# Kernel tuning notes

Hardware: AMD Instinct MI355X
Metric: run time of the kernel (lower is better)

## Reference

```python
import jax, jax.numpy as jnp
import numpy as np

B, S = 2, 2048
D_MODEL = 1024
N_HEADS = 16
N_VALUES = 8192
D_RETR = 128
MAX_POS = 2048


def setup_inputs() -> dict:
    key = jax.random.key(0)
    ks = jax.random.split(key, 10)
    s = 0.02
    return {
        "hidden_states": jax.random.normal(ks[0], (B, S, D_MODEL), jnp.float32),
        "attention_mask": jnp.ones((B, S), jnp.float32),
        "Wq": jax.random.normal(ks[1], (D_MODEL, D_MODEL), jnp.float32) * s,
        "bq": jnp.zeros((D_MODEL,), jnp.float32),
        "Wk": jax.random.normal(ks[2], (D_MODEL, D_MODEL), jnp.float32) * s,
        "bk": jnp.zeros((D_MODEL,), jnp.float32),
        # torch init is round(ones)=all ones; use random 0/1 so the per-head dynamic mask is exercised
        "dynamic_mask": jnp.round(jax.random.uniform(ks[3], (N_HEADS, MAX_POS), jnp.float32)),
        "Wvq": jax.random.normal(ks[4], (D_MODEL, D_RETR), jnp.float32) * s,
        "bvq": jnp.zeros((D_RETR,), jnp.float32),
        "v_keys": jax.random.normal(ks[5], (N_VALUES, D_RETR), jnp.float32) * s,
        "v_embed": jax.random.normal(ks[6], (N_VALUES, D_MODEL), jnp.float32) * s,
        "Wo": jax.random.normal(ks[7], (D_MODEL, D_MODEL), jnp.float32) * s,
        "bo": jnp.zeros((D_MODEL,), jnp.float32),
    }


def reference(hidden_states, attention_mask, Wq, bq, Wk, bk, dynamic_mask,
              Wvq, bvq, v_keys, v_embed, Wo, bo):
    b, s, d = hidden_states.shape
    h = dynamic_mask.shape[0]
    hd = d // h
    dtype = hidden_states.dtype
    min_d = jnp.finfo(dtype).min

    q = (hidden_states @ Wq + bq).reshape(b, s, h, hd).transpose(0, 2, 1, 3)  # [B,H,S,hd]
    k = (hidden_states @ Wk + bk).reshape(b, s, h, hd).transpose(0, 2, 1, 3)

    # inner_func: top-1 codebook value retrieval
    vq = hidden_states @ Wvq + bvq                      # [B,S,Dr]
    sim = jnp.einsum('bsr,nr->bsn', vq, v_keys)         # [B,S,Nv]
    idx = jnp.argmax(sim, axis=-1)                      # top-1 indices [B,S]
    v = hidden_states * v_embed[idx]                    # [B,S,D]
    v = v.reshape(b, s, h, hd).transpose(0, 2, 1, 3)    # [B,H,S,hd]

    # 4D causal mask fused with per-head dynamic mask and padding mask
    tgt = attention_mask.shape[-1]
    causal = jnp.where(jnp.arange(tgt)[None, :] > jnp.arange(s)[:, None],
                       min_d, jnp.array(0, dtype))[None, None]        # [1,1,S,S]
    am = attention_mask[:, None, None, :] * dynamic_mask[None, :, None, :tgt]  # [B,H,1,S]
    padding = causal + am                                              # [B,H,S,S]
    mask = jnp.where(padding == 0, min_d, causal)                      # [B,H,S,S]

    scores = jnp.einsum('bhqd,bhkd->bhqk', q, k) / jnp.sqrt(jnp.array(hd, dtype))
    scores = scores + mask
    w = jax.nn.softmax(scores.astype(jnp.float32), axis=-1).astype(dtype)

    out = jnp.einsum('bhqk,bhkd->bhqd', w, v)            # [B,H,S,hd]
    out = out.transpose(0, 2, 1, 3).reshape(b, s, d)
    return out @ Wo + bo
```

## Files before the change

kernel.cpp:

```cpp
#include <hip/hip_runtime.h>
#include <hip/hip_bf16.h>
#include <math.h>

#define MIN_D (-3.402823466e+38f)

constexpr int Bb = 2, Ss = 2048, Dm = 1024, Hh = 16, HDd = 64, NV = 8192, DRr = 128;
constexpr int Mrows = Bb * Ss;
constexpr float MARGIN = 0.01f;
constexpr int CAP = 262144;
constexpr float C2 = 0.18033688011112042f;

typedef __attribute__((ext_vector_type(8))) short bf16x8;
typedef __attribute__((ext_vector_type(4))) float f32x4;

__device__ inline unsigned short f2bf(float x) {
    union { float f; unsigned u; } v; v.f = x;
    unsigned r = v.u + 0x7fff + ((v.u >> 16) & 1);
    return (unsigned short)(r >> 16);
}
__device__ inline float bf2f(unsigned short u) {
    union { unsigned u; float f; } v; v.u = ((unsigned)u) << 16;
    return v.f;
}
__device__ inline unsigned pk_bf16(float a, float b) {
    float2 t; t.x = a; t.y = b;
    __hip_bfloat162 h = __float22bfloat162_rn(t);
    return *(unsigned*)&h;
}

__global__ __launch_bounds__(256)
void cvt_bf16(const float* __restrict__ x, unsigned short* __restrict__ y)
{
    size_t i = ((size_t)blockIdx.x * 256 + threadIdx.x) * 8;
    float4 a = *(const float4*)(x + i);
    float4 b = *(const float4*)(x + i + 4);
    uint4 p;
    p.x = pk_bf16(a.x, a.y);
    p.y = pk_bf16(a.z, a.w);
    p.z = pk_bf16(b.x, b.y);
    p.w = pk_bf16(b.z, b.w);
    *(uint4*)(y + i) = p;
}

__global__ __launch_bounds__(256)
void transpose_cvt3(const float* __restrict__ W0, const float* __restrict__ W1,
                    const float* __restrict__ W2, unsigned short* __restrict__ T0,
                    unsigned short* __restrict__ T1, unsigned short* __restrict__ T2)
{
    const float* W = blockIdx.z == 0 ? W0 : (blockIdx.z == 1 ? W1 : W2);
    unsigned short* WT = blockIdx.z == 0 ? T0 : (blockIdx.z == 1 ? T1 : T2);
    __shared__ unsigned short T[64][72];
    const int tid = threadIdx.x;
    const int n0 = blockIdx.x * 64, k0 = blockIdx.y * 64;
    const int rr = tid >> 4, cc = tid & 15;
#pragma unroll
    for (int q2 = 0; q2 < 4; ++q2) {
        int kk = rr * 4 + q2;
        float4 v = *(const float4*)(W + (size_t)(k0 + kk) * Dm + n0 + cc * 4);
        T[cc * 4 + 0][kk] = f2bf(v.x);
        T[cc * 4 + 1][kk] = f2bf(v.y);
        T[cc * 4 + 2][kk] = f2bf(v.z);
        T[cc * 4 + 3][kk] = f2bf(v.w);
    }
    __syncthreads();
#pragma unroll
    for (int q2 = 0; q2 < 4; ++q2) {
        int nn = rr * 4 + q2;
        uint2 u;
        u.x = (unsigned)T[nn][cc * 4 + 0] | ((unsigned)T[nn][cc * 4 + 1] << 16);
        u.y = (unsigned)T[nn][cc * 4 + 2] | ((unsigned)T[nn][cc * 4 + 3] << 16);
        *(uint2*)(WT + (size_t)(n0 + nn) * Dm + k0 + cc * 4) = u;
    }
}

template<bool BF16OUT>
__global__ __launch_bounds__(512)
void gemm_bf16(const unsigned short* __restrict__ A,
               const unsigned short* BT0, const unsigned short* BT1,
               const float* bias0, const float* bias1,
               void* C0, void* C1, int N, int K)
{
    const unsigned short* BT = blockIdx.z ? BT1 : BT0;
    const float* bias = blockIdx.z ? bias1 : bias0;
    void* C = blockIdx.z ? C1 : C0;
    __shared__ __align__(16) unsigned short As[128 * 32];
    __shared__ __align__(16) unsigned short Bs[128 * 32];
    const int tid = threadIdx.x;
    const int l = tid & 63, w = tid >> 6;
    const int l15 = l & 15, l4 = l >> 4;
    const int wm = w >> 2, wn = w & 3;
    const int row0 = blockIdx.y * 128, col0 = blockIdx.x * 128;

    f32x4 acc[4][2];
#pragma unroll
    for (int mi = 0; mi < 4; ++mi)
#pragma unroll
        for (int ni = 0; ni < 2; ++ni) acc[mi][ni] = (f32x4)(0.f);

    for (int k0 = 0; k0 < K; k0 += 32) {
        __syncthreads();
        {
            int r = tid >> 2, pc = tid & 3;
            uint4 vv = *(const uint4*)(A + (size_t)(row0 + r) * K + k0 + pc * 8);
            *(uint4*)&As[tid * 8] = vv;
        }
        {
            int r = tid >> 2, pc = tid & 3;
            uint4 vv = *(const uint4*)(BT + (size_t)(col0 + r) * K + k0 + pc * 8);
            *(uint4*)&Bs[tid * 8] = vv;
        }
        __syncthreads();

        bf16x8 af[4], bf[2];
#pragma unroll
        for (int mi = 0; mi < 4; ++mi)
            af[mi] = *(bf16x8*)&As[(wm * 64 + mi * 16 + l15) * 32 + l4 * 8];
#pragma unroll
        for (int ni = 0; ni < 2; ++ni)
            bf[ni] = *(bf16x8*)&Bs[(wn * 32 + ni * 16 + l15) * 32 + l4 * 8];
#pragma unroll
        for (int mi = 0; mi < 4; ++mi)
#pragma unroll
            for (int ni = 0; ni < 2; ++ni)
                acc[mi][ni] = __builtin_amdgcn_mfma_f32_16x16x32_bf16(af[mi], bf[ni], acc[mi][ni], 0, 0, 0);
    }

#pragma unroll
    for (int mi = 0; mi < 4; ++mi)
#pragma unroll
        for (int ni = 0; ni < 2; ++ni)
#pragma unroll
            for (int j = 0; j < 4; ++j) {
                int row = row0 + wm * 64 + mi * 16 + l4 * 4 + j;
                int col = col0 + wn * 32 + ni * 16 + l15;
                float vv = acc[mi][ni][j] + bias[col];
                if (BF16OUT)
                    ((unsigned short*)C)[(size_t)row * N + col] = f2bf(vv);
                else
                    ((float*)C)[(size_t)row * N + col] = vv;
            }
}

__global__ __launch_bounds__(256)
void gemm_vq_partial(const float* __restrict__ A, const float* __restrict__ W,
                     float* __restrict__ P)
{
    __shared__ float As[64][36];
    __shared__ float Ws[32][64];
    const int tid = threadIdx.x;
    const int row0 = blockIdx.y * 64, col0 = blockIdx.x * 64;
    const int kbase = blockIdx.z * 256;
    const int tr = tid >> 4, tc = tid & 15;
    float acc[4][4] = {};

    for (int k0 = kbase; k0 < kbase + 256; k0 += 32) {
        __syncthreads();
#pragma unroll
        for (int q2 = 0; q2 < 2; ++q2) {
            int oc = q2 * 256 + tid;
            int r = oc >> 3, c4 = (oc & 7) << 2;
            *(float4*)&As[r][c4] = *(const float4*)(A + (size_t)(row0 + r) * Dm + k0 + c4);
        }
#pragma unroll
        for (int q2 = 0; q2 < 2; ++q2) {
            int oc = q2 * 256 + tid;
            int r = oc >> 4, c4 = (oc & 15) << 2;
            *(float4*)&Ws[r][c4] = *(const float4*)(W + (size_t)(k0 + r) * DRr + col0 + c4);
        }
        __syncthreads();
#pragma unroll 8
        for (int kk = 0; kk < 32; ++kk) {
            float a[4];
#pragma unroll
            for (int i = 0; i < 4; ++i) a[i] = As[tr * 4 + i][kk];
            float4 bv = *(const float4*)&Ws[kk][tc * 4];
            float b[4] = {bv.x, bv.y, bv.z, bv.w};
#pragma unroll
            for (int i = 0; i < 4; ++i)
#pragma unroll
                for (int j = 0; j < 4; ++j)
                    acc[i][j] = fmaf(a[i], b[j], acc[i][j]);
        }
    }
    float* Pz = P + (size_t)blockIdx.z * Mrows * DRr;
#pragma unroll
    for (int i = 0; i < 4; ++i) {
        int r = row0 + tr * 4 + i;
        float4 ov = {acc[i][0], acc[i][1], acc[i][2], acc[i][3]};
        *(float4*)(Pz + (size_t)r * DRr + col0 + tc * 4) = ov;
    }
}

__global__ __launch_bounds__(256)
void reduce_vq(const float* __restrict__ P, const float* __restrict__ bias,
               float* __restrict__ vqb, unsigned short* __restrict__ vq_hi)
{
    const size_t i4 = ((size_t)blockIdx.x * 256 + threadIdx.x) * 4;
    const int col = (int)(i4 & 127);
    const size_t stride = (size_t)Mrows * DRr;
    float4 s = *(const float4*)(P + i4);
#pragma unroll
    for (int z = 1; z < 4; ++z) {
        float4 p = *(const float4*)(P + stride * z + i4);
        s.x += p.x; s.y += p.y; s.z += p.z; s.w += p.w;
    }
    float4 bv = *(const float4*)(bias + col);
    s.x += bv.x; s.y += bv.y; s.z += bv.z; s.w += bv.w;
    *(float4*)(vqb + i4) = s;
    uint2 u;
    u.x = pk_bf16(s.x, s.y);
    u.y = pk_bf16(s.z, s.w);
    *(uint2*)(vq_hi + i4) = u;
}

__global__ __launch_bounds__(512)
void sim_gemm0(const unsigned short* __restrict__ A,
               const unsigned short* __restrict__ BT,
               float* __restrict__ rtm)
{
    __shared__ __align__(16) unsigned short As[128 * 32];
    __shared__ __align__(16) unsigned short Bs[128 * 32];
    __shared__ float red[128][4];
    const int tid = threadIdx.x;
    const int l = tid & 63, w = tid >> 6;
    const int l15 = l & 15, l4 = l >> 4;
    const int wm = w >> 2, wn = w & 3;
    const int row0 = blockIdx.y * 128, col0 = blockIdx.x * 128;

    f32x4 acc[4][2];
#pragma unroll
    for (int mi = 0; mi < 4; ++mi)
#pragma unroll
        for (int ni = 0; ni < 2; ++ni) acc[mi][ni] = (f32x4)(0.f);

    for (int k0 = 0; k0 < DRr; k0 += 32) {
        __syncthreads();
        {
            int r = tid >> 2, pc = tid & 3;
            __builtin_amdgcn_global_load_lds(
                (const __attribute__((address_space(1))) unsigned int*)(A + (size_t)(row0 + r) * DRr + k0 + pc * 8),
                (__attribute__((address_space(3))) unsigned int*)&As[tid * 8], 16, 0, 0);
            __builtin_amdgcn_global_load_lds(
                (const __attribute__((address_space(1))) unsigned int*)(BT + (size_t)(col0 + r) * DRr + k0 + pc * 8),
                (__attribute__((address_space(3))) unsigned int*)&Bs[tid * 8], 16, 0, 0);
        }
        __syncthreads();

        bf16x8 af[4], bf[2];
#pragma unroll
        for (int mi = 0; mi < 4; ++mi)
            af[mi] = *(bf16x8*)&As[(wm * 64 + mi * 16 + l15) * 32 + l4 * 8];
#pragma unroll
        for (int ni = 0; ni < 2; ++ni)
            bf[ni] = *(bf16x8*)&Bs[(wn * 32 + ni * 16 + l15) * 32 + l4 * 8];
#pragma unroll
        for (int mi = 0; mi < 4; ++mi)
#pragma unroll
            for (int ni = 0; ni < 2; ++ni)
                acc[mi][ni] = __builtin_amdgcn_mfma_f32_16x16x32_bf16(af[mi], bf[ni], acc[mi][ni], 0, 0, 0);
    }

    float rm[4][4];
#pragma unroll
    for (int mi = 0; mi < 4; ++mi)
#pragma unroll
        for (int j = 0; j < 4; ++j)
            rm[mi][j] = fmaxf(acc[mi][0][j], acc[mi][1][j]);
#pragma unroll
    for (int off = 1; off < 16; off <<= 1)
#pragma unroll
        for (int mi = 0; mi < 4; ++mi)
#pragma unroll
            for (int j = 0; j < 4; ++j)
                rm[mi][j] = fmaxf(rm[mi][j], __shfl_xor(rm[mi][j], off));
    if (l15 == 0) {
#pragma unroll
        for (int mi = 0; mi < 4; ++mi)
#pragma unroll
            for (int j = 0; j < 4; ++j)
                red[wm * 64 + mi * 16 + l4 * 4 + j][wn] = rm[mi][j];
    }
    __syncthreads();
    if (tid < 128) {
        float m = fmaxf(fmaxf(red[tid][0], red[tid][1]),
                        fmaxf(red[tid][2], red[tid][3]));
        rtm[(size_t)blockIdx.x * Mrows + row0 + tid] = m;
    }
}

__global__ __launch_bounds__(256)
void sim_combine2(const float* __restrict__ rtm, float* __restrict__ thr)
{
    int r = blockIdx.x * 256 + threadIdx.x;
    if (r >= Mrows) return;
    float m = -INFINITY;
#pragma unroll 8
    for (int c = 0; c < 64; ++c)
        m = fmaxf(m, rtm[(size_t)c * Mrows + r]);
    thr[r] = m - MARGIN;
}

__global__ __launch_bounds__(256)
void collect_pairs(const float* __restrict__ rtm, const float* __restrict__ thr,
                   unsigned* __restrict__ cnt, unsigned* __restrict__ pairs)
{
    const int idx = blockIdx.x * 256 + threadIdx.x;
    const int tile = idx >> 12, row = idx & 4095;
    const bool pred = rtm[(size_t)tile * Mrows + row] >= thr[row];
    unsigned long long mask = __ballot(pred);
    if (mask) {
        const int lane = threadIdx.x & 63;
        const int leader = __ffsll((long long)mask) - 1;
        unsigned base = 0;
        if (lane == leader) base = atomicAdd(cnt, (unsigned)__popcll(mask));
        base = (unsigned)__shfl((int)base, leader);
        if (pred) {
            unsigned off = (unsigned)__popcll(mask & ((1ull << lane) - 1ull));
            pairs[base + off] = ((unsigned)row << 6) | (unsigned)tile;
        }
    }
}

__global__ __launch_bounds__(256)
void rescore_pair(const unsigned* __restrict__ pairs, const unsigned* __restrict__ cnt,
                  const float* __restrict__ vq, const float* __restrict__ vkeys,
                  unsigned long long* __restrict__ best)
{
    __shared__ float vqs[128];
    __shared__ float part[256];
    const int tid = threadIdx.x;
    const unsigned n = min(*cnt, (unsigned)CAP);
    for (unsigned i = blockIdx.x; i < n; i += gridDim.x) {
        const unsigned p = pairs[i];
        const unsigned row = p >> 6, tile = p & 63u;
        if (tid < 32) {
            float4 v = *(const float4*)(vq + (size_t)row * 128 + tid * 4);
            *(float4*)&vqs[tid * 4] = v;
        }
        __syncthreads();
        const int k = tid & 127, h = (tid >> 7) * 64;
        const float* kp = vkeys + (size_t)(tile * 128 + k) * 128 + h;
        float s = 0.f;
#pragma unroll
        for (int d = 0; d < 64; d += 4) {
            float4 kv = *(const float4*)(kp + d);
            s = fmaf(vqs[h + d + 0], kv.x, s);
            s = fmaf(vqs[h + d + 1], kv.y, s);
            s = fmaf(vqs[h + d + 2], kv.z, s);
            s = fmaf(vqs[h + d + 3], kv.w, s);
        }
        part[tid] = s;
        __syncthreads();
        if (tid < 64) {
            float s0 = part[tid] + part[tid + 128];
            float s1 = part[tid + 64] + part[tid + 192];
            float bs = s0; int bk = tid;
            if (s1 > s0) { bs = s1; bk = tid + 64; }
#pragma unroll
            for (int off = 1; off < 64; off <<= 1) {
                float os = __shfl_xor(bs, off);
                int ok = __shfl_xor(bk, off);
                if (os > bs || (os == bs && ok < bk)) { bs = os; bk = ok; }
            }
            if (tid == 0) {
                unsigned key = tile * 128 + bk;
                unsigned fb = __float_as_uint(bs);
                fb = (fb & 0x80000000u) ? ~fb : (fb | 0x80000000u);
                unsigned long long enc = ((unsigned long long)fb << 32) | (unsigned)(~key);
                atomicMax(best + row, enc);
            }
        }
        __syncthreads();
    }
}

__global__ __launch_bounds__(256)
void build_vt(const float* __restrict__ hs, const float* __restrict__ vembed,
              const unsigned long long* __restrict__ best,
              unsigned short* __restrict__ vt)
{
    __shared__ unsigned short T[64][73];
    __shared__ int ids[64];
    const int tid = threadIdx.x;
    const int kt = blockIdx.x;
    const int bh = blockIdx.y;
    const int b = bh >> 4, h = bh & 15;
    if (tid < 64) {
        int row = b * Ss + kt * 64 + tid;
        ids[tid] = (int)((~(unsigned)(best[row] & 0xFFFFFFFFull)) & 8191u);
    }
    __syncthreads();
    {
        int r = tid >> 2, c16 = (tid & 3) * 16;
        size_t hrow = (size_t)(b * Ss + kt * 64 + r) * Dm + h * HDd + c16;
        size_t erow = (size_t)ids[r] * Dm + h * HDd + c16;
#pragma unroll
        for (int q2 = 0; q2 < 4; ++q2) {
            float4 a = *(const float4*)(hs + hrow + q2 * 4);
            float4 e = *(const float4*)(vembed + erow + q2 * 4);
            T[r][c16 + q2 * 4 + 0] = f2bf(a.x * e.x);
            T[r][c16 + q2 * 4 + 1] = f2bf(a.y * e.y);
            T[r][c16 + q2 * 4 + 2] = f2bf(a.z * e.z);
            T[r][c16 + q2 * 4 + 3] = f2bf(a.w * e.w);
        }
    }
    __syncthreads();
    {
        int d = tid >> 2, kc = (tid & 3) * 16;
        unsigned short ob[16];
#pragma unroll
        for (int i = 0; i < 16; ++i) ob[i] = T[kc + i][d];
        unsigned short* op = vt + ((size_t)(b * Hh + h) * HDd + d) * Ss + kt * 64 + kc;
        *(uint4*)op = *(uint4*)&ob[0];
        *(uint4*)(op + 8) = *(uint4*)&ob[8];
    }
}

__global__ __launch_bounds__(256)
void mean_vt(const unsigned short* __restrict__ vt, float* __restrict__ mv)
{
    const int bh = blockIdx.x;
    const int b = bh >> 4, h = bh & 15;
    const int d = threadIdx.x >> 2, part = threadIdx.x & 3;
    const unsigned short* row = vt + ((size_t)bh * HDd + d) * Ss + part * 512;
    float s = 0.f;
    for (int j = 0; j < 512; j += 8) {
        uint4 u = *(const uint4*)(row + j);
        const unsigned uu[4] = {u.x, u.y, u.z, u.w};
#pragma unroll
        for (int m = 0; m < 4; ++m) {
            s += bf2f((unsigned short)(uu[m] & 0xffff));
            s += bf2f((unsigned short)(uu[m] >> 16));
        }
    }
    s += __shfl_xor(s, 1);
    s += __shfl_xor(s, 2);
    if (part == 0) mv[b * Dm + h * HDd + d] = s * (1.f / 2048.f);
}

__global__ __launch_bounds__(512)
void attn_mfma4(const unsigned short* __restrict__ q, const unsigned short* __restrict__ k,
                const unsigned short* __restrict__ vt, const float* __restrict__ am,
                const float* __restrict__ dmask, const float* __restrict__ meanv,
                unsigned short* __restrict__ o)
{
    __shared__ __align__(16) unsigned char smem[40960];
    __shared__ float uniflag[128];
    unsigned char* Ksm = smem;
    unsigned char* Vsm = smem + 8192;
    unsigned char* Psm = smem + 16384;
    float* amdmf = (float*)(smem + 32768);

    const int tid = threadIdx.x;
    const int l = tid & 63, w = tid >> 6;
    const int l15 = l & 15, l4 = l >> 4;
    const int lin = blockIdx.x + (blockIdx.y << 4) + (blockIdx.z << 8);
    const int half = lin >> 8, rem = lin & 255;
    const int qtb = rem & 15;
    const int qt = half ? (15 - qtb) : qtb;
    const int h = rem >> 4;
    const int b = half;
    const int row0 = qt * 128;

    {
        int j = tid * 4;
        float4 a = *(const float4*)(am + b * Ss + j);
        float4 d = *(const float4*)(dmask + h * Ss + j);
        float4 m;
        m.x = (a.x * d.x == 0.f) ? MIN_D : 0.f;
        m.y = (a.y * d.y == 0.f) ? MIN_D : 0.f;
        m.z = (a.z * d.z == 0.f) ? MIN_D : 0.f;
        m.w = (a.w * d.w == 0.f) ? MIN_D : 0.f;
        *(float4*)&amdmf[j] = m;
    }

    const int qloc = w * 16 + l15;
    const int qrow = row0 + qloc;
    bf16x8 qf[2];
    {
        const unsigned short* qp = q + ((size_t)(b * Ss + qrow)) * Dm + h * HDd + l4 * 8;
        qf[0] = *(const bf16x8*)qp;
        qf[1] = *(const bf16x8*)(qp + 32);
    }

    f32x4 acc[4];
#pragma unroll
    for (int d2 = 0; d2 < 4; ++d2) acc[d2] = (f32x4)(0.f);
    float mrun = -INFINITY, lrun = 0.f;
    const int ktmax = 2 * qt + 1;

    for (int kt = 0; kt <= ktmax; ++kt) {
        __syncthreads();
        {
            int key = tid >> 3, pc = tid & 7, lc = pc ^ (key & 7);
            uint4 vv = *(const uint4*)(k + ((size_t)(b * Ss + kt * 64 + key)) * Dm
                                       + h * HDd + lc * 8);
            *(uint4*)&Ksm[tid * 16] = vv;
        }
        {
            int d = tid >> 3, pc = tid & 7, lc = pc ^ (d & 7);
            uint4 vv = *(const uint4*)(vt + ((size_t)(b * Hh + h) * HDd + d) * Ss
                                       + kt * 64 + lc * 8);
            *(uint4*)&Vsm[tid * 16] = vv;
        }
        __syncthreads();

        f32x4 sreg[4];
#pragma unroll
        for (int kb = 0; kb < 4; ++kb) {
            const int key16 = kb * 16 + l15;
            const int sw = key16 & 7;
            bf16x8 k0 = *(bf16x8*)&Ksm[key16 * 128 + ((l4 ^ sw) * 16)];
            bf16x8 k1 = *(bf16x8*)&Ksm[key16 * 128 + (((4 + l4) ^ sw) * 16)];
            f32x4 s = (f32x4)(0.f);
            s = __builtin_amdgcn_mfma_f32_16x16x32_bf16(k0, qf[0], s, 0, 0, 0);
            s = __builtin_amdgcn_mfma_f32_16x16x32_bf16(k1, qf[1], s, 0, 0, 0);
            sreg[kb] = s;
        }

        float sv[16];
#pragma unroll
        for (int kb = 0; kb < 4; ++kb)
#pragma unroll
            for (int r = 0; r < 4; ++r) {
                const int key = kt * 64 + kb * 16 + l4 * 4 + r;
                const float mval = (key > qrow) ? MIN_D : amdmf[key];
                sv[kb * 4 + r] = fmaf(sreg[kb][r], C2, mval);
            }

        float pm = fmaxf(fmaxf(sv[0], sv[1]), sv[2]);
        pm = fmaxf(fmaxf(pm, sv[3]), fmaxf(sv[4], sv[5]));
        pm = fmaxf(fmaxf(pm, sv[6]), fmaxf(sv[7], sv[8]));
        pm = fmaxf(fmaxf(pm, sv[9]), fmaxf(sv[10], sv[11]));
        pm = fmaxf(fmaxf(pm, sv[12]), fmaxf(sv[13], sv[14]));
        pm = fmaxf(pm, sv[15]);
        pm = fmaxf(pm, __shfl_xor(pm, 16));
        pm = fmaxf(pm, __shfl_xor(pm, 32));

        if (__any(pm > mrun + 8.f)) {
            const float mn = fmaxf(mrun, pm);
            const float sc = __builtin_amdgcn_exp2f(mrun - mn);
            lrun *= sc;
#pragma unroll
            for (int d2 = 0; d2 < 4; ++d2) acc[d2] *= sc;
            mrun = mn;
        }

        float p[16], rs = 0.f;
#pragma unroll
        for (int i = 0; i < 16; ++i) {
            p[i] = __builtin_amdgcn_exp2f(sv[i] - mrun);
            rs += p[i];
        }
        rs += __shfl_xor(rs, 16);
        rs += __shfl_xor(rs, 32);
        lrun += rs;

        const unsigned pswz = (l15 & 7) << 4;
#pragma unroll
        for (int kb = 0; kb < 4; ++kb) {
            uint2 u;
            u.x = pk_bf16(p[kb * 4 + 0], p[kb * 4 + 1]);
            u.y = pk_bf16(p[kb * 4 + 2], p[kb * 4 + 3]);
            *(uint2*)&Psm[qloc * 128 + ((kb * 32 + l4 * 8) ^ pswz)] = u;
        }

#pragma unroll
        for (int ks = 0; ks < 2; ++ks) {
            bf16x8 pa = *(bf16x8*)&Psm[qloc * 128 + ((ks * 64 + l4 * 16) ^ pswz)];
#pragma unroll
            for (int d2 = 0; d2 < 4; ++d2) {
                const int dd = d2 * 16 + l15;
                bf16x8 vb = *(bf16x8*)&Vsm[dd * 128 + ((ks * 64 + l4 * 16) ^ ((dd & 7) << 4))];
                acc[d2] = __builtin_amdgcn_mfma_f32_16x16x32_bf16(vb, pa, acc[d2], 0, 0, 0);
            }
        }
    }

    const float inv = 1.f / lrun;
    const bool uni = (mrun <= -1e37f);
    __syncthreads();
    unsigned short* stg = (unsigned short*)smem;
    uniflag[qloc] = uni ? 1.f : 0.f;
#pragma unroll
    for (int d2 = 0; d2 < 4; ++d2) {
        uint2 u;
        u.x = pk_bf16(acc[d2][0] * inv, acc[d2][1] * inv);
        u.y = pk_bf16(acc[d2][2] * inv, acc[d2][3] * inv);
        *(uint2*)&stg[qloc * 72 + d2 * 16 + l4 * 4] = u;
    }
    __syncthreads();
    {
        const int r = tid >> 2, c16 = (tid & 3) * 16;
        const bool u = uniflag[r] != 0.f;
        uint4 o0, o1;
        if (u) {
            unsigned short ob[16];
#pragma unroll
            for (int i = 0; i < 16; ++i)
                ob[i] = f2bf(meanv[b * Dm + h * HDd + c16 + i]);
            o0 = *(uint4*)&ob[0];
            o1 = *(uint4*)&ob[8];
        } else {
            o0 = *(uint4*)&stg[r * 72 + c16];
            o1 = *(uint4*)&stg[r * 72 + c16 + 8];
        }
        unsigned short* op = o + ((size_t)(b * Ss + row0 + r)) * Dm + h * HDd + c16;
        *(uint4*)op = o0;
        *(uint4*)(op + 8) = o1;
    }
}

extern "C" void kernel_launch(void* const* d_in, const int* in_sizes, int n_in,
                              void* d_out, int out_size, void* d_ws, size_t ws_size,
                              hipStream_t stream)
{
    const float* hs     = (const float*)d_in[0];
    const float* amask  = (const float*)d_in[1];
    const float* Wq     = (const float*)d_in[2];
    const float* bq     = (const float*)d_in[3];
    const float* Wk     = (const float*)d_in[4];
    const float* bk     = (const float*)d_in[5];
    const float* dmask  = (const float*)d_in[6];
    const float* Wvq    = (const float*)d_in[7];
    const float* bvq    = (const float*)d_in[8];
    const float* vkeys  = (const float*)d_in[9];
    const float* vembed = (const float*)d_in[10];
    const float* Wo     = (const float*)d_in[11];
    const float* bo     = (const float*)d_in[12];
    float* out = (float*)d_out;

    char* w = (char*)d_ws;
    size_t off = 0;
    auto take = [&](size_t n) { char* p = w + off; off = (off + n + 255) & ~(size_t)255; return p; };
    unsigned short* hsbf  = (unsigned short*)take((size_t)Mrows * Dm * 2);
    unsigned short* WqT   = (unsigned short*)take((size_t)Dm * Dm * 2);
    unsigned short* WkT   = (unsigned short*)take((size_t)Dm * Dm * 2);
    unsigned short* WoT   = (unsigned short*)take((size_t)Dm * Dm * 2);
    unsigned short* qbf   = (unsigned short*)take((size_t)Mrows * Dm * 2);
    unsigned short* kbf   = (unsigned short*)take((size_t)Mrows * Dm * 2);
    unsigned short* vtb   = (unsigned short*)take((size_t)Mrows * Dm * 2);
    unsigned short* attno = (unsigned short*)take((size_t)Mrows * Dm * 2);
    float* vqp   = (float*)take((size_t)4 * Mrows * DRr * 4);
    float* vqb   = (float*)take((size_t)Mrows * DRr * 4);
    unsigned short* vq_hi = (unsigned short*)take((size_t)Mrows * DRr * 2);
    unsigned short* vk_hi = (unsigned short*)take((size_t)NV * DRr * 2);
    float* rtm   = (float*)take((size_t)64 * Mrows * 4);
    float* thr   = (float*)take((size_t)Mrows * 4);
    unsigned* cnt = (unsigned*)take(256);
    unsigned* pairs = (unsigned*)take((size_t)CAP * 4);
    unsigned long long* best = (unsigned long long*)take((size_t)Mrows * 8);
    float* mvb   = (float*)take((size_t)Bb * Dm * 4);

    hipMemsetAsync(cnt, 0, 4, stream);
    hipMemsetAsync(best, 0, (size_t)Mrows * 8, stream);

    dim3 blk(256);
    cvt_bf16<<<dim3(Mrows * Dm / 2048), blk, 0, stream>>>(hs, hsbf);
    transpose_cvt3<<<dim3(Dm / 64, Dm / 64, 3), blk, 0, stream>>>(Wq, Wk, Wo, WqT, WkT, WoT);
    gemm_bf16<true><<<dim3(Dm / 128, Mrows / 128, 2), dim3(512), 0, stream>>>(
        hsbf, WqT, WkT, bq, bk, qbf, kbf, Dm, Dm);
    gemm_vq_partial<<<dim3(DRr / 64, Mrows / 64, 4), blk, 0, stream>>>(hs, Wvq, vqp);
    reduce_vq<<<dim3(Mrows * DRr / 1024), blk, 0, stream>>>(vqp, bvq, vqb, vq_hi);
    cvt_bf16<<<dim3(NV * DRr / 2048), blk, 0, stream>>>(vkeys, vk_hi);
    sim_gemm0<<<dim3(NV / 128, Mrows / 128), dim3(512), 0, stream>>>(vq_hi, vk_hi, rtm);
    sim_combine2<<<dim3(Mrows / 256), blk, 0, stream>>>(rtm, thr);
    collect_pairs<<<dim3(64 * Mrows / 256), blk, 0, stream>>>(rtm, thr, cnt, pairs);
    rescore_pair<<<dim3(2048), blk, 0, stream>>>(pairs, cnt, vqb, vkeys, best);
    build_vt<<<dim3(Ss / 64, Bb * Hh), blk, 0, stream>>>(hs, vembed, best, vtb);
    mean_vt<<<dim3(Bb * Hh), blk, 0, stream>>>(vtb, mvb);
    attn_mfma4<<<dim3(Ss / 128, Hh, Bb), dim3(512), 0, stream>>>(
        qbf, kbf, vtb, amask, dmask, mvb, attno);
    gemm_bf16<false><<<dim3(Dm / 128, Mrows / 128, 1), dim3(512), 0, stream>>>(
        attno, WoT, WoT, bo, bo, out, out, Dm, Dm);
}
```

Baseline: 292.7 us.

## Double-buffer K/V tiles in attention and restructure sim GEMM with register-resident queries

The attention kernel now prefetches the next K and V tiles into registers while the current tile is computed, then writes them into a second shared-memory buffer, so there is one barrier per iteration instead of two. The similarity kernel is rewritten so each block keeps its query fragments in registers across the whole 128-wide inner dimension. It streams 512 keys through double-buffered, XOR-swizzled shared memory, emitting a max per 128-key chunk so the rtm layout stays the same. This is meant to hide global-load latency and cut synchronisation, at the cost of more shared memory per block (lower possible occupancy) and more registers.

Result: faster. 276.5 us (-5.5%).

```diff
diff --git a/kernel.cpp b/kernel.cpp
--- a/kernel.cpp
+++ b/kernel.cpp
@@ -214,77 +214,90 @@
 }
 
 __global__ __launch_bounds__(512)
-void sim_gemm0(const unsigned short* __restrict__ A,
-               const unsigned short* __restrict__ BT,
-               float* __restrict__ rtm)
-{
-    __shared__ __align__(16) unsigned short As[128 * 32];
-    __shared__ __align__(16) unsigned short Bs[128 * 32];
-    __shared__ float red[128][4];
+void sim_max(const unsigned short* __restrict__ vq_hi,
+             const unsigned short* __restrict__ vk_hi,
+             float* __restrict__ rtm)
+{
+    __shared__ __align__(16) unsigned short Buf[2][64 * 128];
     const int tid = threadIdx.x;
     const int l = tid & 63, w = tid >> 6;
     const int l15 = l & 15, l4 = l >> 4;
-    const int wm = w >> 2, wn = w & 3;
-    const int row0 = blockIdx.y * 128, col0 = blockIdx.x * 128;
-
-    f32x4 acc[4][2];
-#pragma unroll
-    for (int mi = 0; mi < 4; ++mi)
-#pragma unroll
-        for (int ni = 0; ni < 2; ++ni) acc[mi][ni] = (f32x4)(0.f);
-
-    for (int k0 = 0; k0 < DRr; k0 += 32) {
-        __syncthreads();
-        {
-            int r = tid >> 2, pc = tid & 3;
-            __builtin_amdgcn_global_load_lds(
-                (const __attribute__((address_space(1))) unsigned int*)(A + (size_t)(row0 + r) * DRr + k0 + pc * 8),
-                (__attribute__((address_space(3))) unsigned int*)&As[tid * 8], 16, 0, 0);
-            __builtin_amdgcn_global_load_lds(
-                (const __attribute__((address_space(1))) unsigned int*)(BT + (size_t)(col0 + r) * DRr + k0 + pc * 8),
-                (__attribute__((address_space(3))) unsigned int*)&Bs[tid * 8], 16, 0, 0);
-        }
-        __syncthreads();
-
-        bf16x8 af[4], bf[2];
-#pragma unroll
-        for (int mi = 0; mi < 4; ++mi)
-            af[mi] = *(bf16x8*)&As[(wm * 64 + mi * 16 + l15) * 32 + l4 * 8];
-#pragma unroll
-        for (int ni = 0; ni < 2; ++ni)
-            bf[ni] = *(bf16x8*)&Bs[(wn * 32 + ni * 16 + l15) * 32 + l4 * 8];
-#pragma unroll
-        for (int mi = 0; mi < 4; ++mi)
-#pragma unroll
-            for (int ni = 0; ni < 2; ++ni)
-                acc[mi][ni] = __builtin_amdgcn_mfma_f32_16x16x32_bf16(af[mi], bf[ni], acc[mi][ni], 0, 0, 0);
-    }
-
-    float rm[4][4];
-#pragma unroll
-    for (int mi = 0; mi < 4; ++mi)
+    const int row0 = blockIdx.y * 128;
+    const int key0 = blockIdx.x * 512;
+
+    bf16x8 af[4];
+    {
+        const unsigned short* ap = vq_hi + (size_t)(row0 + w * 16 + l15) * 128 + l4 * 8;
+#pragma unroll
+        for (int kk = 0; kk < 4; ++kk) af[kk] = *(const bf16x8*)(ap + kk * 32);
+    }
+
+#pragma unroll
+    for (int q2 = 0; q2 < 2; ++q2) {
+        int oc = q2 * 512 + tid;
+        int r = oc >> 4, pc = oc & 15;
+        int lc = pc ^ (r & 15);
+        uint4 vv = *(const uint4*)(vk_hi + (size_t)(key0 + r) * 128 + lc * 8);
+        *(uint4*)&Buf[0][oc * 8] = vv;
+    }
+    __syncthreads();
+
+    float tmax[4];
+
+    for (int t = 0; t < 8; ++t) {
+        const int cur = t & 1;
+        uint4 st[2];
+        if (t + 1 < 8) {
+#pragma unroll
+            for (int q2 = 0; q2 < 2; ++q2) {
+                int oc = q2 * 512 + tid;
+                int r = oc >> 4, pc = oc & 15;
+                int lc = pc ^ (r & 15);
+                st[q2] = *(const uint4*)(vk_hi + (size_t)(key0 + (t + 1) * 64 + r) * 128 + lc * 8);
+            }
+        }
+        f32x4 acc[4];
+#pragma unroll
+        for (int ni = 0; ni < 4; ++ni) {
+            const int key16 = ni * 16 + l15;
+            bf16x8 bfr[4];
+#pragma unroll
+            for (int kk = 0; kk < 4; ++kk)
+                bfr[kk] = *(bf16x8*)&Buf[cur][key16 * 128 + (((kk * 4 + l4) ^ (key16 & 15)) * 8)];
+            f32x4 a = (f32x4)(0.f);
+#pragma unroll
+            for (int kk = 0; kk < 4; ++kk)
+                a = __builtin_amdgcn_mfma_f32_16x16x32_bf16(af[kk], bfr[kk], a, 0, 0, 0);
+            acc[ni] = a;
+        }
+        float tm[4];
 #pragma unroll
         for (int j = 0; j < 4; ++j)
-            rm[mi][j] = fmaxf(acc[mi][0][j], acc[mi][1][j]);
-#pragma unroll
-    for (int off = 1; off < 16; off <<= 1)
-#pragma unroll
-        for (int mi = 0; mi < 4; ++mi)
+            tm[j] = fmaxf(fmaxf(acc[0][j], acc[1][j]), fmaxf(acc[2][j], acc[3][j]));
+#pragma unroll
+        for (int off = 1; off < 16; off <<= 1)
 #pragma unroll
             for (int j = 0; j < 4; ++j)
-                rm[mi][j] = fmaxf(rm[mi][j], __shfl_xor(rm[mi][j], off));
-    if (l15 == 0) {
-#pragma unroll
-        for (int mi = 0; mi < 4; ++mi)
-#pragma unroll
-            for (int j = 0; j < 4; ++j)
-                red[wm * 64 + mi * 16 + l4 * 4 + j][wn] = rm[mi][j];
-    }
-    __syncthreads();
-    if (tid < 128) {
-        float m = fmaxf(fmaxf(red[tid][0], red[tid][1]),
-                        fmaxf(red[tid][2], red[tid][3]));
-        rtm[(size_t)blockIdx.x * Mrows + row0 + tid] = m;
+                tm[j] = fmaxf(tm[j], __shfl_xor(tm[j], off));
+        if ((t & 1) == 0) {
+#pragma unroll
+            for (int j = 0; j < 4; ++j) tmax[j] = tm[j];
+        } else {
+            if (l15 == 0) {
+                const size_t tbase = (size_t)(blockIdx.x * 4 + (t >> 1)) * Mrows;
+#pragma unroll
+                for (int j = 0; j < 4; ++j)
+                    rtm[tbase + row0 + w * 16 + l4 * 4 + j] = fmaxf(tmax[j], tm[j]);
+            }
+        }
+        if (t + 1 < 8) {
+#pragma unroll
+            for (int q2 = 0; q2 < 2; ++q2) {
+                int oc = q2 * 512 + tid;
+                *(uint4*)&Buf[cur ^ 1][oc * 8] = st[q2];
+            }
+        }
+        __syncthreads();
     }
 }
 
@@ -439,17 +452,15 @@
 }
 
 __global__ __launch_bounds__(512)
-void attn_mfma4(const unsigned short* __restrict__ q, const unsigned short* __restrict__ k,
+void attn_mfma5(const unsigned short* __restrict__ q, const unsigned short* __restrict__ k,
                 const unsigned short* __restrict__ vt, const float* __restrict__ am,
                 const float* __restrict__ dmask, const float* __restrict__ meanv,
                 unsigned short* __restrict__ o)
 {
-    __shared__ __align__(16) unsigned char smem[40960];
+    __shared__ __align__(16) unsigned char smem[57344];
     __shared__ float uniflag[128];
-    unsigned char* Ksm = smem;
-    unsigned char* Vsm = smem + 8192;
-    unsigned char* Psm = smem + 16384;
-    float* amdmf = (float*)(smem + 32768);
+    unsigned char* Psm = smem + 32768;
+    float* amdmf = (float*)(smem + 49152);
 
     const int tid = threadIdx.x;
     const int l = tid & 63, w = tid >> 6;
@@ -483,6 +494,19 @@
         qf[1] = *(const bf16x8*)(qp + 32);
     }
 
+    const int skey = tid >> 3, spc = tid & 7;
+    const int slk = spc ^ (skey & 7);
+    const int svd = tid >> 3;
+    const int slv = spc ^ (svd & 7);
+
+    {
+        uint4 kv = *(const uint4*)(k + ((size_t)(b * Ss + skey)) * Dm + h * HDd + slk * 8);
+        *(uint4*)&smem[tid * 16] = kv;
+        uint4 vv = *(const uint4*)(vt + ((size_t)(b * Hh + h) * HDd + svd) * Ss + slv * 8);
+        *(uint4*)&smem[16384 + tid * 16] = vv;
+    }
+    __syncthreads();
+
     f32x4 acc[4];
 #pragma unroll
     for (int d2 = 0; d2 < 4; ++d2) acc[d2] = (f32x4)(0.f);
@@ -490,20 +514,16 @@
     const int ktmax = 2 * qt + 1;
 
     for (int kt = 0; kt <= ktmax; ++kt) {
-        __syncthreads();
-        {
-            int key = tid >> 3, pc = tid & 7, lc = pc ^ (key & 7);
-            uint4 vv = *(const uint4*)(k + ((size_t)(b * Ss + kt * 64 + key)) * Dm
-                                       + h * HDd + lc * 8);
-            *(uint4*)&Ksm[tid * 16] = vv;
-        }
-        {
-            int d = tid >> 3, pc = tid & 7, lc = pc ^ (d & 7);
-            uint4 vv = *(const uint4*)(vt + ((size_t)(b * Hh + h) * HDd + d) * Ss
-                                       + kt * 64 + lc * 8);
-            *(uint4*)&Vsm[tid * 16] = vv;
-        }
-        __syncthreads();
+        const unsigned cb = (unsigned)(kt & 1) << 13;
+        unsigned char* Ksm = smem + cb;
+        unsigned char* Vsm = smem + 16384 + cb;
+        uint4 kst, vst;
+        if (kt < ktmax) {
+            kst = *(const uint4*)(k + ((size_t)(b * Ss + (kt + 1) * 64 + skey)) * Dm
+                                  + h * HDd + slk * 8);
+            vst = *(const uint4*)(vt + ((size_t)(b * Hh + h) * HDd + svd) * Ss
+                                  + (kt + 1) * 64 + slv * 8);
+        }
 
         f32x4 sreg[4];
 #pragma unroll
@@ -575,11 +595,17 @@
                 acc[d2] = __builtin_amdgcn_mfma_f32_16x16x32_bf16(vb, pa, acc[d2], 0, 0, 0);
             }
         }
+
+        if (kt < ktmax) {
+            const unsigned nb = cb ^ 8192u;
+            *(uint4*)&smem[nb + tid * 16] = kst;
+            *(uint4*)&smem[16384 + nb + tid * 16] = vst;
+        }
+        __syncthreads();
     }
 
     const float inv = 1.f / lrun;
     const bool uni = (mrun <= -1e37f);
-    __syncthreads();
     unsigned short* stg = (unsigned short*)smem;
     uniflag[qloc] = uni ? 1.f : 0.f;
 #pragma unroll
@@ -652,8 +678,8 @@
     unsigned long long* best = (unsigned long long*)take((size_t)Mrows * 8);
     float* mvb   = (float*)take((size_t)Bb * Dm * 4);
 
-    hipMemsetAsync(cnt, 0, 4, stream);
-    hipMemsetAsync(best, 0, (size_t)Mrows * 8, stream);
+    (void)hipMemsetAsync(cnt, 0, 4, stream);
+    (void)hipMemsetAsync(best, 0, (size_t)Mrows * 8, stream);
 
     dim3 blk(256);
     cvt_bf16<<<dim3(Mrows * Dm / 2048), blk, 0, stream>>>(hs, hsbf);
@@ -663,13 +689,13 @@
     gemm_vq_partial<<<dim3(DRr / 64, Mrows / 64, 4), blk, 0, stream>>>(hs, Wvq, vqp);
     reduce_vq<<<dim3(Mrows * DRr / 1024), blk, 0, stream>>>(vqp, bvq, vqb, vq_hi);
     cvt_bf16<<<dim3(NV * DRr / 2048), blk, 0, stream>>>(vkeys, vk_hi);
-    sim_gemm0<<<dim3(NV / 128, Mrows / 128), dim3(512), 0, stream>>>(vq_hi, vk_hi, rtm);
+    sim_max<<<dim3(NV / 512, Mrows / 128), dim3(512), 0, stream>>>(vq_hi, vk_hi, rtm);
     sim_combine2<<<dim3(Mrows / 256), blk, 0, stream>>>(rtm, thr);
     collect_pairs<<<dim3(64 * Mrows / 256), blk, 0, stream>>>(rtm, thr, cnt, pairs);
     rescore_pair<<<dim3(2048), blk, 0, stream>>>(pairs, cnt, vqb, vkeys, best);
     build_vt<<<dim3(Ss / 64, Bb * Hh), blk, 0, stream>>>(hs, vembed, best, vtb);
     mean_vt<<<dim3(Bb * Hh), blk, 0, stream>>>(vtb, mvb);
-    attn_mfma4<<<dim3(Ss / 128, Hh, Bb), dim3(512), 0, stream>>>(
+    attn_mfma5<<<dim3(Ss / 128, Hh, Bb), dim3(512), 0, stream>>>(
         qbf, kbf, vtb, amask, dmask, mvb, attno);
     gemm_bf16<false><<<dim3(Dm / 128, Mrows / 128, 1), dim3(512), 0, stream>>>(
         attno, WoT, WoT, bo, bo, out, out, Dm, Dm);
```
